# Optimization experiments

Measured on AMD Instinct MI355X. Metric: run time of the kernel, lower is better.

Reference implementation:

```python
import jax, jax.numpy as jnp
import numpy as np

NUM_HEADS = 16
H_DIM = 1024
HEAD_DIM = H_DIM // NUM_HEADS  # 64
B, S = 8, 1024


def setup_inputs() -> dict:
    key = jax.random.key(0)
    ks = jax.random.split(key, 8)
    query = jax.random.normal(ks[0], (B, S, H_DIM), dtype=jnp.float32)
    key_t = jax.random.normal(ks[1], (B, S, H_DIM), dtype=jnp.float32)
    value = jax.random.normal(ks[2], (B, S, H_DIM), dtype=jnp.float32)
    attn_mask = jnp.ones((B, S, S), dtype=jnp.int32)
    # Per-head projection weights, stacked: [H, h_dim, head_dim]
    sc = 1.0 / np.sqrt(H_DIM)
    Wq = jax.random.normal(ks[3], (NUM_HEADS, H_DIM, HEAD_DIM), dtype=jnp.float32) * sc
    Wk = jax.random.normal(ks[4], (NUM_HEADS, H_DIM, HEAD_DIM), dtype=jnp.float32) * sc
    Wv = jax.random.normal(ks[5], (NUM_HEADS, H_DIM, HEAD_DIM), dtype=jnp.float32) * sc
    Wo = jax.random.normal(ks[6], (H_DIM, H_DIM), dtype=jnp.float32) * sc
    return {"query": query, "key": key_t, "value": value, "attn_mask": attn_mask,
            "Wq": Wq, "Wk": Wk, "Wv": Wv, "Wo": Wo}


def reference(query, key, value, attn_mask, Wq, Wk, Wv, Wo):
    scale = 1.0 / jnp.sqrt(jnp.float32(HEAD_DIM))  # from DotProductAttention.build
    # Fused per-head projections: [B,S,D] x [H,D,K] -> [B,H,S,K]
    q = jnp.einsum('bsd,hdk->bhsk', query, Wq)
    k = jnp.einsum('bsd,hdk->bhsk', key, Wk)
    v = jnp.einsum('bsd,hdk->bhsk', value, Wv)
    # Scores [B,H,S,S]; masked_fill where mask==0 (applied before scaling,
    # matching original; -inf * scale stays -inf)
    score = jnp.einsum('bhqk,bhmk->bhqm', q, k)
    mask = attn_mask[:, None, :, :]  # broadcast over heads
    score = jnp.where(mask == 0, -jnp.inf, score)
    p = jax.nn.softmax(score * scale, axis=-1)
    head = jnp.einsum('bhqm,bhmk->bhqk', p, v)  # [B,H,S,K]
    # Concat heads along feature dim: [B,S,H*K]
    concat = head.transpose(0, 2, 1, 3).reshape(B, S, H_DIM)
    return concat @ Wo
```

## Files before the change

kernel.cpp:

```cpp
#include <hip/hip_runtime.h>
#include <stdint.h>


typedef unsigned short u16;
typedef __attribute__((ext_vector_type(8))) short bf16x8;
typedef __attribute__((ext_vector_type(4))) float f32x4;
typedef __attribute__((ext_vector_type(4))) short short4_t;

#define MFMA16(a, b, c) __builtin_amdgcn_mfma_f32_16x16x32_bf16((a), (b), (c), 0, 0, 0)

__device__ __forceinline__ u16 f2bf(float f) {
  union { float f; uint32_t u; } v; v.f = f;
  uint32_t r = v.u + 0x7fffu + ((v.u >> 16) & 1u);
  return (u16)(r >> 16);
}
__device__ __forceinline__ u16 f2bf_fast(float f) {
  union { float f; uint32_t u; } v; v.f = f;
  return (u16)((v.u + 0x8000u) >> 16);
}

__device__ __forceinline__ void async16(const u16* g, u16* l) {
  __builtin_amdgcn_global_load_lds(
      (const __attribute__((address_space(1))) void*)g,
      (__attribute__((address_space(3))) void*)l, 16, 0, 0);
}

__device__ __forceinline__ void gemm_core(u16* As, u16* Bs, const u16* A,
                                          const u16* Bt, u16* C, float* Cf,
                                          int m0, int n0, int mode) {
  const int tid = threadIdx.x;
  const int lane = tid & 63;
  const int w = tid >> 6;
  const int wm = w >> 1, wn = w & 1;
  const int rA = lane >> 2;
  const int cA = (lane & 3) * 8;
  const int m_l = lane & 15;
  const int koff = (lane >> 4) * 8;

  f32x4 acc[4][4];
#pragma unroll
  for (int i = 0; i < 4; i++)
#pragma unroll
    for (int j = 0; j < 4; j++) acc[i][j] = (f32x4){0.f, 0.f, 0.f, 0.f};

  const u16* a0 = A + (size_t)(m0 + (2 * w + 0) * 16 + rA) * 1024 + cA;
  const u16* a1 = A + (size_t)(m0 + (2 * w + 1) * 16 + rA) * 1024 + cA;
  const u16* b0 = Bt + (size_t)(n0 + (2 * w + 0) * 16 + rA) * 1024 + cA;
  const u16* b1 = Bt + (size_t)(n0 + (2 * w + 1) * 16 + rA) * 1024 + cA;
  u16* as0 = &As[(2 * w + 0) * 512];
  u16* as1 = &As[(2 * w + 1) * 512];
  u16* bs0 = &Bs[(2 * w + 0) * 512];
  u16* bs1 = &Bs[(2 * w + 1) * 512];

  for (int k0 = 0; k0 < 1024; k0 += 32) {
    __syncthreads();
    async16(a0 + k0, as0);
    async16(a1 + k0, as1);
    async16(b0 + k0, bs0);
    async16(b1 + k0, bs1);
    __syncthreads();

    bf16x8 af[4], bfr[4];
#pragma unroll
    for (int mt = 0; mt < 4; mt++)
      af[mt] = *(const bf16x8*)&As[(wm * 64 + mt * 16 + m_l) * 32 + koff];
#pragma unroll
    for (int nt = 0; nt < 4; nt++)
      bfr[nt] = *(const bf16x8*)&Bs[(wn * 64 + nt * 16 + m_l) * 32 + koff];
#pragma unroll
    for (int mt = 0; mt < 4; mt++)
#pragma unroll
      for (int nt = 0; nt < 4; nt++)
        acc[mt][nt] = MFMA16(af[mt], bfr[nt], acc[mt][nt]);
  }

  const int quad = lane >> 4;
#pragma unroll
  for (int mt = 0; mt < 4; mt++) {
    int m_base = m0 + wm * 64 + mt * 16 + quad * 4;
    int b = m_base >> 10, s = m_base & 1023;
#pragma unroll
    for (int nt = 0; nt < 4; nt++) {
      int n_g = n0 + wn * 64 + nt * 16 + m_l;
      if (mode == 0) {
        int h = n_g >> 6, d = n_g & 63;
        u16* p = C + ((size_t)(b * 16 + h) * 1024 + s) * 64 + d;
#pragma unroll
        for (int r = 0; r < 4; r++) p[(size_t)r * 64] = f2bf(acc[mt][nt][r]);
      } else if (mode == 1) {
        int h = n_g >> 6, d = n_g & 63;
        u16* p = C + ((size_t)(b * 16 + h) * 64 + d) * 1024 + s;
        short4_t pk;
#pragma unroll
        for (int r = 0; r < 4; r++) pk[r] = (short)f2bf(acc[mt][nt][r]);
        *(short4_t*)p = pk;
      } else {
        float* p = Cf + (size_t)m_base * 1024 + n_g;
#pragma unroll
        for (int r = 0; r < 4; r++) p[(size_t)r * 1024] = acc[mt][nt][r];
      }
    }
  }
}

__global__ __launch_bounds__(256) void qkv_kernel(
    const u16* __restrict__ q, const u16* __restrict__ k,
    const u16* __restrict__ v, const u16* __restrict__ wtq,
    const u16* __restrict__ wtk, const u16* __restrict__ wtv, u16* qb, u16* kb,
    u16* vt) {
  __shared__ u16 As[128 * 32], Bs[128 * 32];
  int z = blockIdx.z;
  const u16* A = (z == 0) ? q : (z == 1) ? k : v;
  const u16* Bt = (z == 0) ? wtq : (z == 1) ? wtk : wtv;
  u16* C = (z == 0) ? qb : (z == 1) ? kb : vt;
  gemm_core(As, Bs, A, Bt, C, nullptr, blockIdx.y * 128, blockIdx.x * 128,
            (z == 2) ? 1 : 0);
}

__global__ __launch_bounds__(256) void out_kernel(const u16* __restrict__ cc,
                                                  const u16* __restrict__ wto,
                                                  float* out) {
  __shared__ u16 As[128 * 32], Bs[128 * 32];
  gemm_core(As, Bs, cc, wto, nullptr, out, blockIdx.y * 128, blockIdx.x * 128,
            2);
}

__global__ void conv_kernel(const float* __restrict__ q,
                            const float* __restrict__ k,
                            const float* __restrict__ v, u16* qc, u16* kc,
                            u16* vc) {
  int z = blockIdx.y;
  size_t t = ((size_t)blockIdx.x * 256 + threadIdx.x) * 4;
  const float* src = (z == 0) ? q : (z == 1) ? k : v;
  u16* dst = (z == 0) ? qc : (z == 1) ? kc : vc;
  float4 f = *(const float4*)(src + t);
  short4_t o;
  o[0] = (short)f2bf(f.x);
  o[1] = (short)f2bf(f.y);
  o[2] = (short)f2bf(f.z);
  o[3] = (short)f2bf(f.w);
  *(short4_t*)(dst + t) = o;
}

__global__ __launch_bounds__(256) void repack_t_kernel(
    const float* __restrict__ Wq, const float* __restrict__ Wk,
    const float* __restrict__ Wv, u16* wtq, u16* wtk, u16* wtv) {
  __shared__ u16 Ts[64 * 66];
  const int h = blockIdx.x, kkt = blockIdx.y, z = blockIdx.z;
  const float* W = (z == 0) ? Wq : (z == 1) ? Wk : Wv;
  u16* O = (z == 0) ? wtq : (z == 1) ? wtk : wtv;
  const int w = threadIdx.x >> 6, lane = threadIdx.x & 63;
#pragma unroll
  for (int i = 0; i < 16; i++) {
    int rr = i * 4 + w;
    float v = W[((size_t)h << 16) + (size_t)(kkt * 64 + rr) * 64 + lane];
    Ts[lane * 66 + rr] = f2bf(v);
  }
  __syncthreads();
#pragma unroll
  for (int i = 0; i < 16; i++) {
    int d = i * 4 + w;
    O[(size_t)(h * 64 + d) * 1024 + kkt * 64 + lane] = Ts[d * 66 + lane];
  }
}

__global__ void repack_wo_kernel(const float* __restrict__ Wo, u16* wto) {
  int t = blockIdx.x * 256 + threadIdx.x;
  int n = t >> 10, kk = t & 1023;
  wto[t] = f2bf(Wo[(kk << 10) + n]);
}

__global__ void pack_mask_kernel(const int* __restrict__ mask,
                                 uint32_t* __restrict__ bits) {
  int t = blockIdx.x * 256 + threadIdx.x;
  unsigned long long bal = __ballot(mask[t] != 0);
  if ((threadIdx.x & 63) == 0) {
    bits[t >> 5] = (uint32_t)bal;
    bits[(t >> 5) + 1] = (uint32_t)(bal >> 32);
  }
}

__global__ __launch_bounds__(256) void attn_kernel(
    const u16* __restrict__ qb, const u16* __restrict__ kb,
    const u16* __restrict__ vt, const uint32_t* __restrict__ mbits,
    u16* __restrict__ cc) {
  __shared__ u16 Ks[64 * 64];
  __shared__ u16 Vs[64 * 64];
  __shared__ u16 Ps[4][32 * 72];

  const int lane = threadIdx.x & 63;
  const int w = threadIdx.x >> 6;
  const int col = lane & 15;
  const int quad = lane >> 4;
  const int h = blockIdx.x, qt = blockIdx.y, b = blockIdx.z;
  const int q0 = qt * 128 + w * 32;
  const size_t bh = (size_t)b * 16 + h;

  const u16* qrow = qb + ((bh << 10) + q0 + col) * 64 + quad * 8;
  bf16x8 qa0 = *(const bf16x8*)qrow;
  bf16x8 qa1 = *(const bf16x8*)(qrow + 32);
  bf16x8 qb0 = *(const bf16x8*)(qrow + 16 * 64);
  bf16x8 qb1 = *(const bf16x8*)(qrow + 16 * 64 + 32);

  const u16* kbase = kb + (bh << 10) * 64;
  const u16* vbase = vt + (bh << 6) * 1024;
  const uint32_t* mrA = mbits + ((size_t)b * 1024 + q0 + col) * 32;
  const uint32_t* mrB = mrA + 16 * 32;
  u16* pwA = Ps[w];
  u16* pwB = Ps[w] + 16 * 72;

  const int LB0 = w * 64, LB1 = (4 + w) * 64;
  const int rS0 = (LB0 + lane) >> 3, cS0 = (lane & 7) ^ (rS0 & 7);
  const int rS1 = (LB1 + lane) >> 3, cS1 = (lane & 7) ^ (rS1 & 7);
  const int sw = col & 7;

  f32x4 O[2][4];
#pragma unroll
  for (int i = 0; i < 2; i++)
#pragma unroll
    for (int j = 0; j < 4; j++) O[i][j] = (f32x4){0.f, 0.f, 0.f, 0.f};
  float vsA = 0.f, vsB = 0.f;
  const float Cs = 0.18033688f;

  for (int kt = 0; kt < 1024; kt += 64) {
    __syncthreads();
    async16(kbase + (size_t)(kt + rS0) * 64 + cS0 * 8, &Ks[LB0 * 8]);
    async16(kbase + (size_t)(kt + rS1) * 64 + cS1 * 8, &Ks[LB1 * 8]);
    async16(vbase + (size_t)rS0 * 1024 + kt + cS0 * 8, &Vs[LB0 * 8]);
    async16(vbase + (size_t)rS1 * 1024 + kt + cS1 * 8, &Vs[LB1 * 8]);
    uint32_t mA0 = mrA[kt >> 5], mA1 = mrA[(kt >> 5) + 1];
    uint32_t mB0 = mrB[kt >> 5], mB1 = mrB[(kt >> 5) + 1];
    __syncthreads();

    bool allset = __all((mA0 & mA1 & mB0 & mB1) == 0xFFFFFFFFu);

#pragma unroll
    for (int st = 0; st < 4; st++) {
      const int krow = st * 16 + col;
      bf16x8 kf0 = *(const bf16x8*)&Ks[krow * 64 + (quad ^ sw) * 8];
      bf16x8 kf1 = *(const bf16x8*)&Ks[krow * 64 + ((4 + quad) ^ sw) * 8];
      const f32x4 z4 = {0.f, 0.f, 0.f, 0.f};
      f32x4 cA = MFMA16(kf0, qa0, z4); cA = MFMA16(kf1, qa1, cA);
      f32x4 cB = MFMA16(kf0, qb0, z4); cB = MFMA16(kf1, qb1, cB);

      float pa[4], pb[4];
#pragma unroll
      for (int r = 0; r < 4; r++) {
        pa[r] = __builtin_amdgcn_exp2f(cA[r] * Cs);
        pb[r] = __builtin_amdgcn_exp2f(cB[r] * Cs);
      }
      if (!allset) {
        uint32_t mwA = (st < 2) ? mA0 : mA1;
        uint32_t mwB = (st < 2) ? mB0 : mB1;
#pragma unroll
        for (int r = 0; r < 4; r++) {
          int bit = (st & 1) * 16 + quad * 4 + r;
          if (!((mwA >> bit) & 1u)) pa[r] = 0.f;
          if (!((mwB >> bit) & 1u)) pb[r] = 0.f;
        }
      }
      short4_t sa, sb;
#pragma unroll
      for (int r = 0; r < 4; r++) {
        vsA += pa[r];
        vsB += pb[r];
        sa[r] = (short)f2bf_fast(pa[r]);
        sb[r] = (short)f2bf_fast(pb[r]);
      }
      *(short4_t*)&pwA[col * 72 + st * 16 + quad * 4] = sa;
      *(short4_t*)&pwB[col * 72 + st * 16 + quad * 4] = sb;
    }

#pragma unroll
    for (int step = 0; step < 2; step++) {
      bf16x8 pfA = *(const bf16x8*)&pwA[col * 72 + step * 32 + quad * 8];
      bf16x8 pfB = *(const bf16x8*)&pwB[col * 72 + step * 32 + quad * 8];
#pragma unroll
      for (int dt = 0; dt < 4; dt++) {
        bf16x8 vf = *(const bf16x8*)&Vs[(dt * 16 + col) * 64 +
                                        ((step * 4 + quad) ^ sw) * 8];
        O[0][dt] = MFMA16(pfA, vf, O[0][dt]);
        O[1][dt] = MFMA16(pfB, vf, O[1][dt]);
      }
    }
  }

  vsA += __shfl_xor(vsA, 16); vsA += __shfl_xor(vsA, 32);
  vsB += __shfl_xor(vsB, 16); vsB += __shfl_xor(vsB, 32);
  float liA[4], liB[4];
#pragma unroll
  for (int r = 0; r < 4; r++) {
    liA[r] = 1.f / __shfl(vsA, quad * 4 + r);
    liB[r] = 1.f / __shfl(vsB, quad * 4 + r);
  }
  u16* crow = cc + ((size_t)b * 1024 + q0) * 1024 + h * 64;
#pragma unroll
  for (int dt = 0; dt < 4; dt++)
#pragma unroll
    for (int r = 0; r < 4; r++) {
      crow[(size_t)(quad * 4 + r) * 1024 + dt * 16 + col] =
          f2bf(O[0][dt][r] * liA[r]);
      crow[(size_t)(16 + quad * 4 + r) * 1024 + dt * 16 + col] =
          f2bf(O[1][dt][r] * liB[r]);
    }
}

extern "C" void kernel_launch(void* const* d_in, const int* in_sizes, int n_in,
                              void* d_out, int out_size, void* d_ws,
                              size_t ws_size, hipStream_t stream) {
  const float* query = (const float*)d_in[0];
  const float* key = (const float*)d_in[1];
  const float* value = (const float*)d_in[2];
  const int* mask = (const int*)d_in[3];
  const float* Wq = (const float*)d_in[4];
  const float* Wk = (const float*)d_in[5];
  const float* Wv = (const float*)d_in[6];
  const float* Wo = (const float*)d_in[7];
  float* out = (float*)d_out;

  u16* wtq = (u16*)d_ws;
  u16* wtk = wtq + (1 << 20);
  u16* wtv = wtk + (1 << 20);
  u16* wto = wtv + (1 << 20);
  u16* qc = wto + (1 << 20);
  u16* kc = qc + (8 << 20);
  u16* vc = kc + (8 << 20);
  u16* qbuf = vc + (8 << 20);
  u16* kbuf = qbuf + (8 << 20);
  u16* vtb = kbuf + (8 << 20);
  uint32_t* mbits = (uint32_t*)(vtb + (8 << 20));
  u16* ccb = qc;

  repack_t_kernel<<<dim3(16, 16, 3), 256, 0, stream>>>(Wq, Wk, Wv, wtq, wtk,
                                                       wtv);
  repack_wo_kernel<<<dim3(4096), 256, 0, stream>>>(Wo, wto);
  conv_kernel<<<dim3(8192, 3), 256, 0, stream>>>(query, key, value, qc, kc,
                                                 vc);
  pack_mask_kernel<<<dim3(32768), 256, 0, stream>>>(mask, mbits);
  qkv_kernel<<<dim3(8, 64, 3), 256, 0, stream>>>(qc, kc, vc, wtq, wtk, wtv,
                                                 qbuf, kbuf, vtb);
  attn_kernel<<<dim3(16, 8, 8), 256, 0, stream>>>(qbuf, kbuf, vtb, mbits, ccb);
  out_kernel<<<dim3(8, 64), 256, 0, stream>>>(ccb, wto, out);
}
```

Baseline: 358.6 us.

## Fuse fp32-to-bf16 input conversion into QKV GEMM with swizzled LDS tiles

```diff
diff --git a/kernel.cpp b/kernel.cpp
--- a/kernel.cpp
+++ b/kernel.cpp
@@ -19,23 +19,22 @@
   return (u16)((v.u + 0x8000u) >> 16);
 }
 
-__device__ __forceinline__ void async16(const u16* g, u16* l) {
+__device__ __forceinline__ void async16(const void* g, void* l) {
   __builtin_amdgcn_global_load_lds(
       (const __attribute__((address_space(1))) void*)g,
       (__attribute__((address_space(3))) void*)l, 16, 0, 0);
 }
 
-__device__ __forceinline__ void gemm_core(u16* As, u16* Bs, const u16* A,
-                                          const u16* Bt, u16* C, float* Cf,
-                                          int m0, int n0, int mode) {
+template <bool AF32>
+__device__ __forceinline__ void gemm_core2(u16* AsRaw, u16* Bs, const void* Av,
+                                           const u16* Bt, u16* C, float* Cf,
+                                           int m0, int n0, int mode) {
   const int tid = threadIdx.x;
   const int lane = tid & 63;
   const int w = tid >> 6;
   const int wm = w >> 1, wn = w & 1;
-  const int rA = lane >> 2;
-  const int cA = (lane & 3) * 8;
   const int m_l = lane & 15;
-  const int koff = (lane >> 4) * 8;
+  const int quad = lane >> 4;
 
   f32x4 acc[4][4];
 #pragma unroll
@@ -43,30 +42,72 @@
 #pragma unroll
     for (int j = 0; j < 4; j++) acc[i][j] = (f32x4){0.f, 0.f, 0.f, 0.f};
 
-  const u16* a0 = A + (size_t)(m0 + (2 * w + 0) * 16 + rA) * 1024 + cA;
-  const u16* a1 = A + (size_t)(m0 + (2 * w + 1) * 16 + rA) * 1024 + cA;
-  const u16* b0 = Bt + (size_t)(n0 + (2 * w + 0) * 16 + rA) * 1024 + cA;
-  const u16* b1 = Bt + (size_t)(n0 + (2 * w + 1) * 16 + rA) * 1024 + cA;
-  u16* as0 = &As[(2 * w + 0) * 512];
-  u16* as1 = &As[(2 * w + 1) * 512];
-  u16* bs0 = &Bs[(2 * w + 0) * 512];
-  u16* bs1 = &Bs[(2 * w + 1) * 512];
+  const int rB = lane >> 2;
+  const int cB = (((lane & 3) ^ ((rB >> 1) & 3))) * 8;
+  const u16* bsrc0 = Bt + (size_t)(n0 + (2 * w + 0) * 16 + rB) * 1024 + cB;
+  const u16* bsrc1 = Bt + (size_t)(n0 + (2 * w + 1) * 16 + rB) * 1024 + cB;
+  u16* bd0 = &Bs[(2 * w + 0) * 16 * 32];
+  u16* bd1 = &Bs[(2 * w + 1) * 16 * 32];
+
+  const float* Af32 = (const float*)Av;
+  const u16* Ab16 = (const u16*)Av;
+  const int rA8 = lane >> 3;
+  const int cA8 = (((lane & 7) ^ (rA8 & 7))) * 4;
+  const float* a32src[4];
+  float* a32dst[4];
+  const u16* a16src0 = Ab16 + (size_t)(m0 + (2 * w + 0) * 16 + rB) * 1024 + cB;
+  const u16* a16src1 = Ab16 + (size_t)(m0 + (2 * w + 1) * 16 + rB) * 1024 + cB;
+  u16* a16d0 = &AsRaw[(2 * w + 0) * 16 * 32];
+  u16* a16d1 = &AsRaw[(2 * w + 1) * 16 * 32];
+  if (AF32) {
+#pragma unroll
+    for (int i = 0; i < 4; i++) {
+      a32src[i] =
+          Af32 + (size_t)(m0 + (4 * w + i) * 8 + rA8) * 1024 + cA8;
+      a32dst[i] = (float*)AsRaw + (4 * w + i) * 8 * 32;
+    }
+  }
 
   for (int k0 = 0; k0 < 1024; k0 += 32) {
     __syncthreads();
-    async16(a0 + k0, as0);
-    async16(a1 + k0, as1);
-    async16(b0 + k0, bs0);
-    async16(b1 + k0, bs1);
+    if (AF32) {
+#pragma unroll
+      for (int i = 0; i < 4; i++) async16(a32src[i] + k0, a32dst[i]);
+    } else {
+      async16(a16src0 + k0, a16d0);
+      async16(a16src1 + k0, a16d1);
+    }
+    async16(bsrc0 + k0, bd0);
+    async16(bsrc1 + k0, bd1);
     __syncthreads();
 
     bf16x8 af[4], bfr[4];
 #pragma unroll
-    for (int mt = 0; mt < 4; mt++)
-      af[mt] = *(const bf16x8*)&As[(wm * 64 + mt * 16 + m_l) * 32 + koff];
-#pragma unroll
-    for (int nt = 0; nt < 4; nt++)
-      bfr[nt] = *(const bf16x8*)&Bs[(wn * 64 + nt * 16 + m_l) * 32 + koff];
+    for (int mt = 0; mt < 4; mt++) {
+      int row = wm * 64 + mt * 16 + m_l;
+      if (AF32) {
+        const float* Af = (const float*)AsRaw;
+        const int s = m_l & 7;
+        f32x4 lo = *(const f32x4*)&Af[row * 32 + ((2 * quad) ^ s) * 4];
+        f32x4 hi = *(const f32x4*)&Af[row * 32 + ((2 * quad + 1) ^ s) * 4];
+        bf16x8 fr;
+#pragma unroll
+        for (int r = 0; r < 4; r++) {
+          fr[r] = (short)f2bf_fast(lo[r]);
+          fr[4 + r] = (short)f2bf_fast(hi[r]);
+        }
+        af[mt] = fr;
+      } else {
+        af[mt] = *(const bf16x8*)&AsRaw[row * 32 +
+                                        (quad ^ ((m_l >> 1) & 3)) * 8];
+      }
+    }
+#pragma unroll
+    for (int nt = 0; nt < 4; nt++) {
+      int row = wn * 64 + nt * 16 + m_l;
+      bfr[nt] =
+          *(const bf16x8*)&Bs[row * 32 + (quad ^ ((m_l >> 1) & 3)) * 8];
+    }
 #pragma unroll
     for (int mt = 0; mt < 4; mt++)
 #pragma unroll
@@ -74,7 +115,6 @@
         acc[mt][nt] = MFMA16(af[mt], bfr[nt], acc[mt][nt]);
   }
 
-  const int quad = lane >> 4;
 #pragma unroll
   for (int mt = 0; mt < 4; mt++) {
     int m_base = m0 + wm * 64 + mt * 16 + quad * 4;
@@ -104,42 +144,26 @@
 }
 
 __global__ __launch_bounds__(256) void qkv_kernel(
-    const u16* __restrict__ q, const u16* __restrict__ k,
-    const u16* __restrict__ v, const u16* __restrict__ wtq,
-    const u16* __restrict__ wtk, const u16* __restrict__ wtv, u16* qb, u16* kb,
-    u16* vt) {
-  __shared__ u16 As[128 * 32], Bs[128 * 32];
+    const float* __restrict__ q, const float* __restrict__ k,
+    const float* __restrict__ v, const u16* __restrict__ wtq,
+    const u16* __restrict__ wtk, const u16* __restrict__ wtv, u16* qb,
+    u16* kb, u16* vt) {
+  __shared__ float Afs[128 * 32];
+  __shared__ u16 Bs[128 * 32];
   int z = blockIdx.z;
-  const u16* A = (z == 0) ? q : (z == 1) ? k : v;
+  const float* A = (z == 0) ? q : (z == 1) ? k : v;
   const u16* Bt = (z == 0) ? wtq : (z == 1) ? wtk : wtv;
   u16* C = (z == 0) ? qb : (z == 1) ? kb : vt;
-  gemm_core(As, Bs, A, Bt, C, nullptr, blockIdx.y * 128, blockIdx.x * 128,
-            (z == 2) ? 1 : 0);
+  gemm_core2<true>((u16*)Afs, Bs, A, Bt, C, nullptr, blockIdx.x * 128,
+                   blockIdx.y * 128, (z == 2) ? 1 : 0);
 }
 
 __global__ __launch_bounds__(256) void out_kernel(const u16* __restrict__ cc,
                                                   const u16* __restrict__ wto,
                                                   float* out) {
   __shared__ u16 As[128 * 32], Bs[128 * 32];
-  gemm_core(As, Bs, cc, wto, nullptr, out, blockIdx.y * 128, blockIdx.x * 128,
-            2);
-}
-
-__global__ void conv_kernel(const float* __restrict__ q,
-                            const float* __restrict__ k,
-                            const float* __restrict__ v, u16* qc, u16* kc,
-                            u16* vc) {
-  int z = blockIdx.y;
-  size_t t = ((size_t)blockIdx.x * 256 + threadIdx.x) * 4;
-  const float* src = (z == 0) ? q : (z == 1) ? k : v;
-  u16* dst = (z == 0) ? qc : (z == 1) ? kc : vc;
-  float4 f = *(const float4*)(src + t);
-  short4_t o;
-  o[0] = (short)f2bf(f.x);
-  o[1] = (short)f2bf(f.y);
-  o[2] = (short)f2bf(f.z);
-  o[3] = (short)f2bf(f.w);
-  *(short4_t*)(dst + t) = o;
+  gemm_core2<false>(As, Bs, cc, wto, nullptr, out, blockIdx.x * 128,
+                    blockIdx.y * 128, 2);
 }
 
 __global__ __launch_bounds__(256) void repack_t_kernel(
@@ -322,23 +346,18 @@
   u16* wtk = wtq + (1 << 20);
   u16* wtv = wtk + (1 << 20);
   u16* wto = wtv + (1 << 20);
-  u16* qc = wto + (1 << 20);
-  u16* kc = qc + (8 << 20);
-  u16* vc = kc + (8 << 20);
-  u16* qbuf = vc + (8 << 20);
+  u16* qbuf = wto + (1 << 20);
   u16* kbuf = qbuf + (8 << 20);
   u16* vtb = kbuf + (8 << 20);
-  uint32_t* mbits = (uint32_t*)(vtb + (8 << 20));
-  u16* ccb = qc;
+  u16* ccb = vtb + (8 << 20);
+  uint32_t* mbits = (uint32_t*)(ccb + (8 << 20));
 
   repack_t_kernel<<<dim3(16, 16, 3), 256, 0, stream>>>(Wq, Wk, Wv, wtq, wtk,
                                                        wtv);
   repack_wo_kernel<<<dim3(4096), 256, 0, stream>>>(Wo, wto);
-  conv_kernel<<<dim3(8192, 3), 256, 0, stream>>>(query, key, value, qc, kc,
-                                                 vc);
   pack_mask_kernel<<<dim3(32768), 256, 0, stream>>>(mask, mbits);
-  qkv_kernel<<<dim3(8, 64, 3), 256, 0, stream>>>(qc, kc, vc, wtq, wtk, wtv,
-                                                 qbuf, kbuf, vtb);
+  qkv_kernel<<<dim3(64, 8, 3), 256, 0, stream>>>(query, key, value, wtq, wtk,
+                                                 wtv, qbuf, kbuf, vtb);
   attn_kernel<<<dim3(16, 8, 8), 256, 0, stream>>>(qbuf, kbuf, vtb, mbits, ccb);
-  out_kernel<<<dim3(8, 64), 256, 0, stream>>>(ccb, wto, out);
-}
+  out_kernel<<<dim3(64, 8), 256, 0, stream>>>(ccb, wto, out);
+}
```

Result: no change. 360.2 us (+0.4%).
